# Optimization experiments

Measured on AMD Instinct MI355X. Metric: run time of the kernel, lower is better.

The kernel has to match this reference:

```python
import jax, jax.numpy as jnp
import numpy as np

B, C, H, W = 32, 64, 32, 32
DIM = H * W          # number of tokens (pixels)
DEPTH = 8
TAU = 1.0
NUM_CLASSES = 10


def setup_inputs() -> dict:
    key = jax.random.key(0)
    ks = jax.random.split(key, 6)
    return {
        "image": jax.random.normal(ks[0], (B, C, H, W), dtype=jnp.float32),
        "WV": 10.0 * jax.random.normal(ks[1], (C, C), dtype=jnp.float32),
        "WK": jax.random.normal(ks[2], (C, C), dtype=jnp.float32),
        "WQ": jax.random.normal(ks[3], (C, C), dtype=jnp.float32),
        "last_W": jax.random.normal(ks[4], (NUM_CLASSES, DIM), dtype=jnp.float32) / np.sqrt(DIM),
        "last_b": jnp.zeros((NUM_CLASSES,), dtype=jnp.float32),
    }


def reference(image, WV, WK, WQ, last_W, last_b):
    # flatten(2).transpose(1,2): (B,C,H,W) -> (B, H*W, C)
    X = image.reshape(B, C, DIM).transpose(0, 2, 1)
    scale = DIM ** (-0.5)
    for _ in range(DEPTH):
        # weight_sharing=True, sign=0 -> W = WV every layer
        Q = X @ WQ                                  # (B, n, C)
        K = X @ WK                                  # (B, n, C)
        scores = jnp.einsum('bnc,bmc->bnm', Q, K) * scale  # (B, n, n)
        A = jax.nn.softmax(scores, axis=-1)
        # diffusion_step (method 'A'): tau * A @ (X @ W) + X
        X = TAU * jnp.einsum('bnm,bmc->bnc', A, X @ WV) + X
    # mean over channel dim -> (B, dim), then Linear(dim, num_classes)
    pred = X.mean(-1) @ last_W.T + last_b
    return pred
```

## Files before the change

### kernel.cpp

```cpp
#include <hip/hip_runtime.h>
#include <math.h>

#define BB    32
#define CCH   64
#define DIMN  1024
#define NCLS  10

typedef __attribute__((ext_vector_type(8))) short bf16x8;
typedef __attribute__((ext_vector_type(4))) float f32x4;
typedef __attribute__((ext_vector_type(4))) unsigned short us4;
typedef __attribute__((ext_vector_type(8))) unsigned short us8;

#define MFMA16(a, b, c) __builtin_amdgcn_mfma_f32_16x16x32_bf16(a, b, c, 0, 0, 0)

__device__ __forceinline__ unsigned short f2bf(float x) {
  unsigned u = __float_as_uint(x);
  unsigned r = u + 0x7fffu + ((u >> 16) & 1u);
  return (unsigned short)(r >> 16);
}
__device__ __forceinline__ float bf2f(unsigned short h) {
  return __uint_as_float(((unsigned)h) << 16);
}
__device__ __forceinline__ void split3(float x, unsigned short& h,
                                       unsigned short& m, unsigned short& l) {
  h = f2bf(x); float hf = bf2f(h);
  float r = x - hf;
  m = f2bf(r); float mf = bf2f(m);
  l = f2bf(r - mf);
}
__device__ __forceinline__ void split3_pk(float x0, float x1,
                                          unsigned& hp, unsigned& mp,
                                          unsigned& lp) {
  unsigned h, m, l;
  asm("v_cvt_pk_bf16_f32 %0, %1, %2" : "=v"(h) : "v"(x0), "v"(x1));
  const float h0 = __uint_as_float(h << 16);
  const float h1 = __uint_as_float(h & 0xffff0000u);
  const float r0 = x0 - h0, r1 = x1 - h1;
  asm("v_cvt_pk_bf16_f32 %0, %1, %2" : "=v"(m) : "v"(r0), "v"(r1));
  const float m0 = __uint_as_float(m << 16);
  const float m1 = __uint_as_float(m & 0xffff0000u);
  asm("v_cvt_pk_bf16_f32 %0, %1, %2" : "=v"(l) : "v"(r0 - m0), "v"(r1 - m1));
  hp = h; mp = m; lp = l;
}
__device__ __forceinline__ void split3_frag(const float* xv, bf16x8& fh,
                                            bf16x8& fm, bf16x8& fl) {
  union U { bf16x8 v; unsigned d[4]; } uh, um, ul;
  #pragma unroll
  for (int p = 0; p < 4; ++p)
    split3_pk(xv[2 * p], xv[2 * p + 1], uh.d[p], um.d[p], ul.d[p]);
  fh = uh.v; fm = um.v; fl = ul.v;
}
__device__ __forceinline__ bf16x8 ld16B(const unsigned short* p) {
  union { us8 u; bf16x8 v; } c;
  c.u = *(const us8*)p;
  return c.v;
}

__global__ __launch_bounds__(256) void k_transpose(const float* __restrict__ img,
                                                   float* __restrict__ X) {
  __shared__ float tile[64][65];
  const int b  = blockIdx.y;
  const int n0 = blockIdx.x * 64;
  const int tx = threadIdx.x & 63;
  const int ty = threadIdx.x >> 6;
  const float* src = img + (size_t)b * CCH * DIMN;
  #pragma unroll
  for (int c = ty; c < 64; c += 4)
    tile[c][tx] = src[(size_t)c * DIMN + n0 + tx];
  __syncthreads();
  float* dst = X + (size_t)b * DIMN * CCH;
  #pragma unroll
  for (int nn = ty; nn < 64; nn += 4)
    dst[(size_t)(n0 + nn) * CCH + tx] = tile[tx][nn];
}

__global__ __launch_bounds__(256) void k_qkv_split(
    const float* __restrict__ X,
    const float* __restrict__ WQ, const float* __restrict__ WK,
    const float* __restrict__ WV,
    float* __restrict__ Q,
    unsigned short* __restrict__ Kh, unsigned short* __restrict__ Km,
    unsigned short* __restrict__ Kl,
    unsigned short* __restrict__ VhT, unsigned short* __restrict__ VmT,
    unsigned short* __restrict__ VlT) {
  __shared__ float xs[16][64];
  __shared__ unsigned short vs[3][16][64];
  const int c  = threadIdx.x & 63;
  const int tg = threadIdx.x >> 6;
  const size_t t0 = (size_t)blockIdx.x * 16;
  #pragma unroll
  for (int r = tg; r < 16; r += 4)
    xs[r][c] = X[(t0 + r) * 64 + c];
  __syncthreads();
  float qa[4] = {0.f,0.f,0.f,0.f};
  float ka[4] = {0.f,0.f,0.f,0.f};
  float va[4] = {0.f,0.f,0.f,0.f};
  for (int j = 0; j < 64; ++j) {
    const float wq = WQ[j * 64 + c];
    const float wk = WK[j * 64 + c];
    const float wv = WV[j * 64 + c];
    #pragma unroll
    for (int r = 0; r < 4; ++r) {
      const float x = xs[tg * 4 + r][j];
      qa[r] = fmaf(x, wq, qa[r]);
      ka[r] = fmaf(x, wk, ka[r]);
      va[r] = fmaf(x, wv, va[r]);
    }
  }
  #pragma unroll
  for (int r = 0; r < 4; ++r) {
    const int t = tg * 4 + r;
    const size_t idx = (t0 + t) * 64 + c;
    Q[idx] = qa[r];
    unsigned short h, m, l;
    split3(ka[r], h, m, l);
    Kh[idx] = h; Km[idx] = m; Kl[idx] = l;
    split3(va[r], h, m, l);
    vs[0][t][c] = h; vs[1][t][c] = m; vs[2][t][c] = l;
  }
  __syncthreads();
  {
    const int row  = threadIdx.x >> 2;
    const int part = threadIdx.x & 3;
    const size_t bofs = (t0 >> 10) * ((size_t)DIMN * 64);
    const size_t kt   = (t0 & 1023) >> 5;
    const size_t tin  = (size_t)part * 8 + ((t0 & 31) >> 2);
    unsigned short* dst[3] = {VhT, VmT, VlT};
    #pragma unroll
    for (int term = 0; term < 3; ++term) {
      us4 pk;
      #pragma unroll
      for (int i = 0; i < 4; ++i) pk[i] = vs[term][part * 4 + i][row];
      *(us4*)&dst[term][bofs + kt * 2048 + (size_t)row * 32 + tin] = pk;
    }
  }
}

__global__ __launch_bounds__(256) void k_qkv_merge(
    float* __restrict__ X,
    const float* __restrict__ Mp, const float* __restrict__ Lp,
    const float* __restrict__ Op,
    const float* __restrict__ WQ, const float* __restrict__ WK,
    const float* __restrict__ WV,
    float* __restrict__ Q,
    unsigned short* __restrict__ Kh, unsigned short* __restrict__ Km,
    unsigned short* __restrict__ Kl,
    unsigned short* __restrict__ VhT, unsigned short* __restrict__ VmT,
    unsigned short* __restrict__ VlT) {
  __shared__ float xs[16][64];
  __shared__ unsigned short vs[3][16][64];
  const int c  = threadIdx.x & 63;
  const int tg = threadIdx.x >> 6;
  const size_t t0 = (size_t)blockIdx.x * 16;
  #pragma unroll
  for (int r = tg; r < 16; r += 4) {
    const size_t grow = t0 + r;
    const float m0 = Mp[grow], m1 = Mp[32768 + grow];
    const float l0 = Lp[grow], l1 = Lp[32768 + grow];
    const float mm = fmaxf(m0, m1);
    const float w0 = __expf(m0 - mm), w1 = __expf(m1 - mm);
    const float inv = 1.0f / (l0 * w0 + l1 * w1);
    const float o0 = Op[grow * 64 + c];
    const float o1 = Op[(size_t)2097152 + grow * 64 + c];
    const float xn = X[grow * 64 + c] + (o0 * w0 + o1 * w1) * inv;
    X[grow * 64 + c] = xn;
    xs[r][c] = xn;
  }
  __syncthreads();
  float qa[4] = {0.f,0.f,0.f,0.f};
  float ka[4] = {0.f,0.f,0.f,0.f};
  float va[4] = {0.f,0.f,0.f,0.f};
  for (int j = 0; j < 64; ++j) {
    const float wq = WQ[j * 64 + c];
    const float wk = WK[j * 64 + c];
    const float wv = WV[j * 64 + c];
    #pragma unroll
    for (int r = 0; r < 4; ++r) {
      const float x = xs[tg * 4 + r][j];
      qa[r] = fmaf(x, wq, qa[r]);
      ka[r] = fmaf(x, wk, ka[r]);
      va[r] = fmaf(x, wv, va[r]);
    }
  }
  #pragma unroll
  for (int r = 0; r < 4; ++r) {
    const int t = tg * 4 + r;
    const size_t idx = (t0 + t) * 64 + c;
    Q[idx] = qa[r];
    unsigned short h, m, l;
    split3(ka[r], h, m, l);
    Kh[idx] = h; Km[idx] = m; Kl[idx] = l;
    split3(va[r], h, m, l);
    vs[0][t][c] = h; vs[1][t][c] = m; vs[2][t][c] = l;
  }
  __syncthreads();
  {
    const int row  = threadIdx.x >> 2;
    const int part = threadIdx.x & 3;
    const size_t bofs = (t0 >> 10) * ((size_t)DIMN * 64);
    const size_t kt   = (t0 & 1023) >> 5;
    const size_t tin  = (size_t)part * 8 + ((t0 & 31) >> 2);
    unsigned short* dst[3] = {VhT, VmT, VlT};
    #pragma unroll
    for (int term = 0; term < 3; ++term) {
      us4 pk;
      #pragma unroll
      for (int i = 0; i < 4; ++i) pk[i] = vs[term][part * 4 + i][row];
      *(us4*)&dst[term][bofs + kt * 2048 + (size_t)row * 32 + tin] = pk;
    }
  }
}

__global__ __launch_bounds__(256, 4) void k_attn_sk(
    const float* __restrict__ Qg,
    const unsigned short* __restrict__ Kh, const unsigned short* __restrict__ Km,
    const unsigned short* __restrict__ Kl,
    const unsigned short* __restrict__ VhT, const unsigned short* __restrict__ VmT,
    const unsigned short* __restrict__ VlT,
    float* __restrict__ Mp, float* __restrict__ Lp, float* __restrict__ Op) {
  __shared__ __align__(16) unsigned short Khs[32 * 72];
  __shared__ __align__(16) unsigned short Kms[32 * 72];
  __shared__ __align__(16) unsigned short Kls[32 * 72];
  __shared__ __align__(16) unsigned short Vhs[64 * 40];
  __shared__ __align__(16) unsigned short Vms[64 * 40];
  __shared__ __align__(16) unsigned short Vls[64 * 40];

  const int tid  = threadIdx.x;
  const int w    = tid >> 6;
  const int lane = tid & 63;
  const int ln   = lane & 15;
  const int q    = lane >> 4;

  const int bid   = blockIdx.x;
  const int xcd   = bid & 7;
  const int seq   = bid >> 3;
  const int b     = xcd * 4 + (seq >> 5);
  const int local = seq & 31;
  const int half  = local >> 4;
  const int i0    = (local & 15) * 64;

  const size_t base = (size_t)b * (DIMN * 64);
  const float scale = 0.03125f;

  const int kj = tid >> 3, kg = tid & 7;
  const int vc = tid >> 2, vg = tid & 3;
  const int klo = kj * 72 + kg * 8;
  const int vlo = vc * 40 + vg * 8;

  bf16x8 qh[2], qm[2], ql[2];
  {
    const int mrow = i0 + 16 * w + ln;
    const float* qp = Qg + base + (size_t)mrow * 64 + 8 * q;
    #pragma unroll
    for (int s = 0; s < 2; ++s) {
      const float4 x0 = ((const float4*)(qp + 32 * s))[0];
      const float4 x1 = ((const float4*)(qp + 32 * s))[1];
      const float xv[8] = {x0.x, x0.y, x0.z, x0.w, x1.x, x1.y, x1.z, x1.w};
      split3_frag(xv, qh[s], qm[s], ql[s]);
    }
  }

  f32x4 O[4];
  #pragma unroll
  for (int ct = 0; ct < 4; ++ct) O[ct] = (f32x4){0.f, 0.f, 0.f, 0.f};
  float m_run = -INFINITY;
  float l_run = 0.f;

  const int kt0 = half * 16;
  for (int kt = kt0; kt < kt0 + 16; ++kt) {
    __syncthreads();

    {
      const size_t tof = base + (size_t)kt * 2048 + tid * 8;
      const us8 a0 = *(const us8*)&Kh[tof];
      const us8 a1 = *(const us8*)&Km[tof];
      const us8 a2 = *(const us8*)&Kl[tof];
      const us8 b0 = *(const us8*)&VhT[tof];
      const us8 b1 = *(const us8*)&VmT[tof];
      const us8 b2 = *(const us8*)&VlT[tof];
      *(us8*)&Khs[klo] = a0;
      *(us8*)&Kms[klo] = a1;
      *(us8*)&Kls[klo] = a2;
      *(us8*)&Vhs[vlo] = b0;
      *(us8*)&Vms[vlo] = b1;
      *(us8*)&Vls[vlo] = b2;
    }
    __syncthreads();

    f32x4 sacc[2];
    #pragma unroll
    for (int ct = 0; ct < 2; ++ct) {
      f32x4 a = (f32x4){0.f, 0.f, 0.f, 0.f};
      #pragma unroll
      for (int s = 0; s < 2; ++s) {
        const int ko = (16 * ct + ln) * 72 + 32 * s + 8 * q;
        const bf16x8 bh = ld16B(&Khs[ko]);
        const bf16x8 bm = ld16B(&Kms[ko]);
        const bf16x8 bl = ld16B(&Kls[ko]);
        a = MFMA16(bh, ql[s], a);
        a = MFMA16(bl, qh[s], a);
        a = MFMA16(bm, qm[s], a);
        a = MFMA16(bh, qm[s], a);
        a = MFMA16(bm, qh[s], a);
        a = MFMA16(bh, qh[s], a);
      }
      sacc[ct] = a;
    }

    float m8 = fmaxf(fmaxf(fmaxf(sacc[0][0], sacc[0][1]),
                           fmaxf(sacc[0][2], sacc[0][3])),
                     fmaxf(fmaxf(sacc[1][0], sacc[1][1]),
                           fmaxf(sacc[1][2], sacc[1][3])));
    m8 = fmaxf(m8, __shfl_xor(m8, 16, 64));
    m8 = fmaxf(m8, __shfl_xor(m8, 32, 64));
    const float mnew  = fmaxf(m_run, m8 * scale);
    const float alpha = __expf(m_run - mnew);
    m_run = mnew;

    float pv[8];
    float s8 = 0.f;
    #pragma unroll
    for (int ct = 0; ct < 2; ++ct) {
      #pragma unroll
      for (int r = 0; r < 4; ++r) {
        const float p = __expf(sacc[ct][r] * scale - m_run);
        pv[ct * 4 + r] = p;
        s8 += p;
      }
    }
    float sr = s8 + __shfl_xor(s8, 16, 64);
    sr = sr + __shfl_xor(sr, 32, 64);
    l_run = l_run * alpha + sr;

    const int srcb = (lane & 48) + ((lane & 48) >> 2);
    float arow[4];
    #pragma unroll
    for (int r = 0; r < 4; ++r) arow[r] = __shfl(alpha, srcb + r, 64);
    #pragma unroll
    for (int ct = 0; ct < 4; ++ct) {
      #pragma unroll
      for (int r = 0; r < 4; ++r) O[ct][r] *= arow[r];
    }

    bf16x8 ph, pm, pl;
    split3_frag(pv, ph, pm, pl);

    #pragma unroll
    for (int ct = 0; ct < 4; ++ct) {
      const int vo = (16 * ct + ln) * 40 + 8 * q;
      const bf16x8 vvh = ld16B(&Vhs[vo]);
      const bf16x8 vvm = ld16B(&Vms[vo]);
      const bf16x8 vvl = ld16B(&Vls[vo]);
      O[ct] = MFMA16(ph, vvh, O[ct]);
      O[ct] = MFMA16(ph, vvm, O[ct]);
      O[ct] = MFMA16(pm, vvh, O[ct]);
      O[ct] = MFMA16(pm, vvm, O[ct]);
      O[ct] = MFMA16(ph, vvl, O[ct]);
      O[ct] = MFMA16(pl, vvh, O[ct]);
    }
  }

  const size_t hofs = (size_t)half * (32 * 1024);
  #pragma unroll
  for (int r = 0; r < 4; ++r) {
    const int row = i0 + 16 * w + 4 * q + r;
    const size_t grow = hofs + (size_t)b * DIMN + row;
    #pragma unroll
    for (int ct = 0; ct < 4; ++ct)
      Op[grow * 64 + ln + 16 * ct] = O[ct][r];
  }
  if (q == 0) {
    const size_t tgrow = hofs + (size_t)b * DIMN + i0 + 16 * w + ln;
    Mp[tgrow] = m_run;
    Lp[tgrow] = l_run;
  }
}

__global__ __launch_bounds__(256) void k_merge_mean(
    const float* __restrict__ X,
    const float* __restrict__ Mp, const float* __restrict__ Lp,
    const float* __restrict__ Op, float* __restrict__ meanv) {
  const int c  = threadIdx.x & 63;
  const int tg = threadIdx.x >> 6;
  const size_t t0 = (size_t)blockIdx.x * 128;
  for (int i = tg; i < 128; i += 4) {
    const size_t grow = t0 + i;
    const float m0 = Mp[grow], m1 = Mp[32768 + grow];
    const float l0 = Lp[grow], l1 = Lp[32768 + grow];
    const float mm = fmaxf(m0, m1);
    const float w0 = __expf(m0 - mm), w1 = __expf(m1 - mm);
    const float inv = 1.0f / (l0 * w0 + l1 * w1);
    const float o0 = Op[grow * 64 + c];
    const float o1 = Op[(size_t)2097152 + grow * 64 + c];
    float v = X[grow * 64 + c] + (o0 * w0 + o1 * w1) * inv;
    #pragma unroll
    for (int off = 32; off > 0; off >>= 1)
      v += __shfl_down(v, off, 64);
    if (c == 0) meanv[grow] = v * (1.0f / 64.0f);
  }
}

__global__ __launch_bounds__(256) void k_head2(
    const float* __restrict__ meanv, const float* __restrict__ lW,
    const float* __restrict__ lb, float* __restrict__ out) {
  __shared__ float red[256];
  const int b   = blockIdx.x;
  const int tid = threadIdx.x;
  float acc[NCLS];
  #pragma unroll
  for (int k = 0; k < NCLS; ++k) acc[k] = 0.f;
  for (int n = tid; n < DIMN; n += 256) {
    const float m = meanv[(size_t)b * DIMN + n];
    #pragma unroll
    for (int k = 0; k < NCLS; ++k)
      acc[k] = fmaf(m, lW[k * DIMN + n], acc[k]);
  }
  for (int k = 0; k < NCLS; ++k) {
    red[tid] = acc[k];
    __syncthreads();
    for (int s = 128; s > 0; s >>= 1) {
      if (tid < s) red[tid] += red[tid + s];
      __syncthreads();
    }
    if (tid == 0) out[b * NCLS + k] = red[0] + lb[k];
    __syncthreads();
  }
}

__global__ __launch_bounds__(256) void k_attn_s(
    const float* __restrict__ Qg,
    const unsigned short* __restrict__ Kh, const unsigned short* __restrict__ Km,
    const unsigned short* __restrict__ Kl,
    const unsigned short* __restrict__ VhT, const unsigned short* __restrict__ VmT,
    const unsigned short* __restrict__ VlT,
    float* __restrict__ X, float* __restrict__ meanout) {
  __shared__ __align__(16) unsigned short Khs[32 * 72];
  __shared__ __align__(16) unsigned short Kms[32 * 72];
  __shared__ __align__(16) unsigned short Kls[32 * 72];
  __shared__ __align__(16) unsigned short Vhs[64 * 40];
  __shared__ __align__(16) unsigned short Vms[64 * 40];
  __shared__ __align__(16) unsigned short Vls[64 * 40];

  const int tid  = threadIdx.x;
  const int w    = tid >> 6;
  const int lane = tid & 63;
  const int ln   = lane & 15;
  const int q    = lane >> 4;
  const int bid = blockIdx.x;
  const int xcd = bid & 7;
  const int seq = bid >> 3;
  const int b   = xcd * 4 + (seq >> 4);
  const int i0  = (seq & 15) * 64;
  const size_t base = (size_t)b * (DIMN * 64);
  const float scale = 0.03125f;

  const int kj = tid >> 3, kg = tid & 7;
  const int vc = tid >> 2, vg = tid & 3;
  const int klo = kj * 72 + kg * 8;
  const int vlo = vc * 40 + vg * 8;

  bf16x8 qh[2], qm[2], ql[2];
  {
    const int mrow = i0 + 16 * w + ln;
    const float* qp = Qg + base + (size_t)mrow * 64 + 8 * q;
    #pragma unroll
    for (int s = 0; s < 2; ++s) {
      const float4 x0 = ((const float4*)(qp + 32 * s))[0];
      const float4 x1 = ((const float4*)(qp + 32 * s))[1];
      const float xv[8] = {x0.x, x0.y, x0.z, x0.w, x1.x, x1.y, x1.z, x1.w};
      split3_frag(xv, qh[s], qm[s], ql[s]);
    }
  }

  f32x4 O[4];
  #pragma unroll
  for (int ct = 0; ct < 4; ++ct) O[ct] = (f32x4){0.f, 0.f, 0.f, 0.f};
  float m_run = -INFINITY;
  float l_run = 0.f;

  for (int kt = 0; kt < 32; ++kt) {
    __syncthreads();
    {
      const size_t tof = base + (size_t)kt * 2048 + tid * 8;
      const us8 a0 = *(const us8*)&Kh[tof];
      const us8 a1 = *(const us8*)&Km[tof];
      const us8 a2 = *(const us8*)&Kl[tof];
      const us8 b0 = *(const us8*)&VhT[tof];
      const us8 b1 = *(const us8*)&VmT[tof];
      const us8 b2 = *(const us8*)&VlT[tof];
      *(us8*)&Khs[klo] = a0;
      *(us8*)&Kms[klo] = a1;
      *(us8*)&Kls[klo] = a2;
      *(us8*)&Vhs[vlo] = b0;
      *(us8*)&Vms[vlo] = b1;
      *(us8*)&Vls[vlo] = b2;
    }
    __syncthreads();

    f32x4 sacc[2];
    #pragma unroll
    for (int ct = 0; ct < 2; ++ct) {
      f32x4 a = (f32x4){0.f, 0.f, 0.f, 0.f};
      #pragma unroll
      for (int s = 0; s < 2; ++s) {
        const int ko = (16 * ct + ln) * 72 + 32 * s + 8 * q;
        const bf16x8 bh = ld16B(&Khs[ko]);
        const bf16x8 bm = ld16B(&Kms[ko]);
        const bf16x8 bl = ld16B(&Kls[ko]);
        a = MFMA16(bh, ql[s], a);
        a = MFMA16(bl, qh[s], a);
        a = MFMA16(bm, qm[s], a);
        a = MFMA16(bh, qm[s], a);
        a = MFMA16(bm, qh[s], a);
        a = MFMA16(bh, qh[s], a);
      }
      sacc[ct] = a;
    }

    float m8 = fmaxf(fmaxf(fmaxf(sacc[0][0], sacc[0][1]),
                           fmaxf(sacc[0][2], sacc[0][3])),
                     fmaxf(fmaxf(sacc[1][0], sacc[1][1]),
                           fmaxf(sacc[1][2], sacc[1][3])));
    m8 = fmaxf(m8, __shfl_xor(m8, 16, 64));
    m8 = fmaxf(m8, __shfl_xor(m8, 32, 64));
    const float mnew  = fmaxf(m_run, m8 * scale);
    const float alpha = __expf(m_run - mnew);
    m_run = mnew;

    float pv[8];
    float s8 = 0.f;
    #pragma unroll
    for (int ct = 0; ct < 2; ++ct) {
      #pragma unroll
      for (int r = 0; r < 4; ++r) {
        const float p = __expf(sacc[ct][r] * scale - m_run);
        pv[ct * 4 + r] = p;
        s8 += p;
      }
    }
    float sr = s8 + __shfl_xor(s8, 16, 64);
    sr = sr + __shfl_xor(sr, 32, 64);
    l_run = l_run * alpha + sr;

    const int srcb = (lane & 48) + ((lane & 48) >> 2);
    float arow[4];
    #pragma unroll
    for (int r = 0; r < 4; ++r) arow[r] = __shfl(alpha, srcb + r, 64);
    #pragma unroll
    for (int ct = 0; ct < 4; ++ct) {
      #pragma unroll
      for (int r = 0; r < 4; ++r) O[ct][r] *= arow[r];
    }

    bf16x8 ph, pm, pl;
    split3_frag(pv, ph, pm, pl);

    #pragma unroll
    for (int ct = 0; ct < 4; ++ct) {
      const int vo = (16 * ct + ln) * 40 + 8 * q;
      const bf16x8 vvh = ld16B(&Vhs[vo]);
      const bf16x8 vvm = ld16B(&Vms[vo]);
      const bf16x8 vvl = ld16B(&Vls[vo]);
      O[ct] = MFMA16(ph, vvh, O[ct]);
      O[ct] = MFMA16(ph, vvm, O[ct]);
      O[ct] = MFMA16(pm, vvh, O[ct]);
      O[ct] = MFMA16(pm, vvm, O[ct]);
      O[ct] = MFMA16(ph, vvl, O[ct]);
      O[ct] = MFMA16(pl, vvh, O[ct]);
    }
  }

  const int srcb = (lane & 48) + ((lane & 48) >> 2);
  float linv[4];
  #pragma unroll
  for (int r = 0; r < 4; ++r) linv[r] = 1.0f / __shfl(l_run, srcb + r, 64);
  #pragma unroll
  for (int r = 0; r < 4; ++r) {
    const int row = i0 + 16 * w + 4 * q + r;
    float srow = 0.f;
    #pragma unroll
    for (int ct = 0; ct < 4; ++ct) {
      float* xp = X + base + (size_t)row * 64 + ln + 16 * ct;
      const float nv = *xp + O[ct][r] * linv[r];
      *xp = nv;
      srow += nv;
    }
    if (meanout) {
      #pragma unroll
      for (int mk = 1; mk <= 8; mk <<= 1)
        srow += __shfl_xor(srow, mk, 64);
      if (ln == 0) meanout[(size_t)b * DIMN + row] = srow * (1.0f / 64.0f);
    }
  }
}

extern "C" void kernel_launch(void* const* d_in, const int* in_sizes, int n_in,
                              void* d_out, int out_size, void* d_ws, size_t ws_size,
                              hipStream_t stream) {
  const float* image = (const float*)d_in[0];
  const float* WV    = (const float*)d_in[1];
  const float* WK    = (const float*)d_in[2];
  const float* WQ    = (const float*)d_in[3];
  const float* lW    = (const float*)d_in[4];
  const float* lb    = (const float*)d_in[5];
  float* out = (float*)d_out;

  float* ws = (float*)d_ws;
  const size_t NELEM = (size_t)BB * DIMN * CCH;
  const size_t NROW  = (size_t)BB * DIMN;

  const size_t need_sk   = (7 * NELEM + 5 * NROW) * sizeof(float);
  const size_t need_fast = (5 * NELEM + NROW) * sizeof(float);

  if (ws_size >= need_sk) {
    float* X = ws;
    float* Q = ws + NELEM;
    unsigned short* Kh  = (unsigned short*)(ws + 2 * NELEM);
    unsigned short* Km  = Kh + NELEM;
    unsigned short* Kl  = Kh + 2 * NELEM;
    unsigned short* VhT = Kh + 3 * NELEM;
    unsigned short* VmT = Kh + 4 * NELEM;
    unsigned short* VlT = Kh + 5 * NELEM;
    float* Op    = ws + 5 * NELEM;
    float* Mp    = ws + 7 * NELEM;
    float* Lp    = Mp + 2 * NROW;
    float* meanv = Lp + 2 * NROW;

    k_transpose<<<dim3(DIMN / 64, BB), 256, 0, stream>>>(image, X);
    k_qkv_split<<<(BB * DIMN) / 16, 256, 0, stream>>>(
        X, WQ, WK, WV, Q, Kh, Km, Kl, VhT, VmT, VlT);
    for (int layer = 0; layer < 8; ++layer) {
      k_attn_sk<<<1024, 256, 0, stream>>>(
          Q, Kh, Km, Kl, VhT, VmT, VlT, Mp, Lp, Op);
      if (layer < 7)
        k_qkv_merge<<<(BB * DIMN) / 16, 256, 0, stream>>>(
            X, Mp, Lp, Op, WQ, WK, WV, Q, Kh, Km, Kl, VhT, VmT, VlT);
    }
    k_merge_mean<<<256, 256, 0, stream>>>(X, Mp, Lp, Op, meanv);
    k_head2<<<BB, 256, 0, stream>>>(meanv, lW, lb, out);
  } else {
    float* X = ws;
    float* Q = ws + NELEM;
    unsigned short* Kh  = (unsigned short*)(ws + 2 * NELEM);
    unsigned short* Km  = Kh + NELEM;
    unsigned short* Kl  = Kh + 2 * NELEM;
    unsigned short* VhT = Kh + 3 * NELEM;
    unsigned short* VmT = Kh + 4 * NELEM;
    unsigned short* VlT = Kh + 5 * NELEM;
    float* meanv = ws + 5 * NELEM;
    (void)need_fast;

    k_transpose<<<dim3(DIMN / 64, BB), 256, 0, stream>>>(image, X);
    for (int layer = 0; layer < 8; ++layer) {
      k_qkv_split<<<(BB * DIMN) / 16, 256, 0, stream>>>(
          X, WQ, WK, WV, Q, Kh, Km, Kl, VhT, VmT, VlT);
      k_attn_s<<<512, 256, 0, stream>>>(
          Q, Kh, Km, Kl, VhT, VmT, VlT, X, (layer == 7) ? meanv : nullptr);
    }
    k_head2<<<BB, 256, 0, stream>>>(meanv, lW, lb, out);
  }
}
```

Before: 716.4 us.

## Load K/V fragments directly from global memory, dropping LDS staging and barriers

Both attention kernels now read the split bf16 K and V tiles straight from global memory into MFMA fragments instead of staging them in shared memory behind two __syncthreads per tile. This removes the LDS round-trip and the per-iteration block barriers. The cost is that each of the four waves fetches the same K/V data separately, relying on L1/L2 caching, and the global loads sit right before the MFMAs that use them, so their latency is harder to hide. k_attn_s also gets a launch-bounds occupancy hint of 4 blocks.

```diff
diff --git a/kernel.cpp b/kernel.cpp
--- a/kernel.cpp
+++ b/kernel.cpp
@@ -218,13 +218,6 @@
     const unsigned short* __restrict__ VhT, const unsigned short* __restrict__ VmT,
     const unsigned short* __restrict__ VlT,
     float* __restrict__ Mp, float* __restrict__ Lp, float* __restrict__ Op) {
-  __shared__ __align__(16) unsigned short Khs[32 * 72];
-  __shared__ __align__(16) unsigned short Kms[32 * 72];
-  __shared__ __align__(16) unsigned short Kls[32 * 72];
-  __shared__ __align__(16) unsigned short Vhs[64 * 40];
-  __shared__ __align__(16) unsigned short Vms[64 * 40];
-  __shared__ __align__(16) unsigned short Vls[64 * 40];
-
   const int tid  = threadIdx.x;
   const int w    = tid >> 6;
   const int lane = tid & 63;
@@ -242,11 +235,6 @@
   const size_t base = (size_t)b * (DIMN * 64);
   const float scale = 0.03125f;
 
-  const int kj = tid >> 3, kg = tid & 7;
-  const int vc = tid >> 2, vg = tid & 3;
-  const int klo = kj * 72 + kg * 8;
-  const int vlo = vc * 40 + vg * 8;
-
   bf16x8 qh[2], qm[2], ql[2];
   {
     const int mrow = i0 + 16 * w + ln;
@@ -268,24 +256,7 @@
 
   const int kt0 = half * 16;
   for (int kt = kt0; kt < kt0 + 16; ++kt) {
-    __syncthreads();
-
-    {
-      const size_t tof = base + (size_t)kt * 2048 + tid * 8;
-      const us8 a0 = *(const us8*)&Kh[tof];
-      const us8 a1 = *(const us8*)&Km[tof];
-      const us8 a2 = *(const us8*)&Kl[tof];
-      const us8 b0 = *(const us8*)&VhT[tof];
-      const us8 b1 = *(const us8*)&VmT[tof];
-      const us8 b2 = *(const us8*)&VlT[tof];
-      *(us8*)&Khs[klo] = a0;
-      *(us8*)&Kms[klo] = a1;
-      *(us8*)&Kls[klo] = a2;
-      *(us8*)&Vhs[vlo] = b0;
-      *(us8*)&Vms[vlo] = b1;
-      *(us8*)&Vls[vlo] = b2;
-    }
-    __syncthreads();
+    const size_t kb = base + (size_t)kt * 2048;
 
     f32x4 sacc[2];
     #pragma unroll
@@ -293,10 +264,10 @@
       f32x4 a = (f32x4){0.f, 0.f, 0.f, 0.f};
       #pragma unroll
       for (int s = 0; s < 2; ++s) {
-        const int ko = (16 * ct + ln) * 72 + 32 * s + 8 * q;
-        const bf16x8 bh = ld16B(&Khs[ko]);
-        const bf16x8 bm = ld16B(&Kms[ko]);
-        const bf16x8 bl = ld16B(&Kls[ko]);
+        const size_t ko = kb + (size_t)(16 * ct + ln) * 64 + 32 * s + 8 * q;
+        const bf16x8 bh = ld16B(&Kh[ko]);
+        const bf16x8 bm = ld16B(&Km[ko]);
+        const bf16x8 bl = ld16B(&Kl[ko]);
         a = MFMA16(bh, ql[s], a);
         a = MFMA16(bl, qh[s], a);
         a = MFMA16(bm, qm[s], a);
@@ -347,10 +318,10 @@
 
     #pragma unroll
     for (int ct = 0; ct < 4; ++ct) {
-      const int vo = (16 * ct + ln) * 40 + 8 * q;
-      const bf16x8 vvh = ld16B(&Vhs[vo]);
-      const bf16x8 vvm = ld16B(&Vms[vo]);
-      const bf16x8 vvl = ld16B(&Vls[vo]);
+      const size_t vo = kb + (size_t)(16 * ct + ln) * 32 + 8 * q;
+      const bf16x8 vvh = ld16B(&VhT[vo]);
+      const bf16x8 vvm = ld16B(&VmT[vo]);
+      const bf16x8 vvl = ld16B(&VlT[vo]);
       O[ct] = MFMA16(ph, vvh, O[ct]);
       O[ct] = MFMA16(ph, vvm, O[ct]);
       O[ct] = MFMA16(pm, vvh, O[ct]);
@@ -427,20 +398,13 @@
   }
 }
 
-__global__ __launch_bounds__(256) void k_attn_s(
+__global__ __launch_bounds__(256, 4) void k_attn_s(
     const float* __restrict__ Qg,
     const unsigned short* __restrict__ Kh, const unsigned short* __restrict__ Km,
     const unsigned short* __restrict__ Kl,
     const unsigned short* __restrict__ VhT, const unsigned short* __restrict__ VmT,
     const unsigned short* __restrict__ VlT,
     float* __restrict__ X, float* __restrict__ meanout) {
-  __shared__ __align__(16) unsigned short Khs[32 * 72];
-  __shared__ __align__(16) unsigned short Kms[32 * 72];
-  __shared__ __align__(16) unsigned short Kls[32 * 72];
-  __shared__ __align__(16) unsigned short Vhs[64 * 40];
-  __shared__ __align__(16) unsigned short Vms[64 * 40];
-  __shared__ __align__(16) unsigned short Vls[64 * 40];
-
   const int tid  = threadIdx.x;
   const int w    = tid >> 6;
   const int lane = tid & 63;
@@ -454,11 +418,6 @@
   const size_t base = (size_t)b * (DIMN * 64);
   const float scale = 0.03125f;
 
-  const int kj = tid >> 3, kg = tid & 7;
-  const int vc = tid >> 2, vg = tid & 3;
-  const int klo = kj * 72 + kg * 8;
-  const int vlo = vc * 40 + vg * 8;
-
   bf16x8 qh[2], qm[2], ql[2];
   {
     const int mrow = i0 + 16 * w + ln;
@@ -479,23 +438,7 @@
   float l_run = 0.f;
 
   for (int kt = 0; kt < 32; ++kt) {
-    __syncthreads();
-    {
-      const size_t tof = base + (size_t)kt * 2048 + tid * 8;
-      const us8 a0 = *(const us8*)&Kh[tof];
-      const us8 a1 = *(const us8*)&Km[tof];
-      const us8 a2 = *(const us8*)&Kl[tof];
-      const us8 b0 = *(const us8*)&VhT[tof];
-      const us8 b1 = *(const us8*)&VmT[tof];
-      const us8 b2 = *(const us8*)&VlT[tof];
-      *(us8*)&Khs[klo] = a0;
-      *(us8*)&Kms[klo] = a1;
-      *(us8*)&Kls[klo] = a2;
-      *(us8*)&Vhs[vlo] = b0;
-      *(us8*)&Vms[vlo] = b1;
-      *(us8*)&Vls[vlo] = b2;
-    }
-    __syncthreads();
+    const size_t kb = base + (size_t)kt * 2048;
 
     f32x4 sacc[2];
     #pragma unroll
@@ -503,10 +446,10 @@
       f32x4 a = (f32x4){0.f, 0.f, 0.f, 0.f};
       #pragma unroll
       for (int s = 0; s < 2; ++s) {
-        const int ko = (16 * ct + ln) * 72 + 32 * s + 8 * q;
-        const bf16x8 bh = ld16B(&Khs[ko]);
-        const bf16x8 bm = ld16B(&Kms[ko]);
-        const bf16x8 bl = ld16B(&Kls[ko]);
+        const size_t ko = kb + (size_t)(16 * ct + ln) * 64 + 32 * s + 8 * q;
+        const bf16x8 bh = ld16B(&Kh[ko]);
+        const bf16x8 bm = ld16B(&Km[ko]);
+        const bf16x8 bl = ld16B(&Kl[ko]);
         a = MFMA16(bh, ql[s], a);
         a = MFMA16(bl, qh[s], a);
         a = MFMA16(bm, qm[s], a);
@@ -557,10 +500,10 @@
 
     #pragma unroll
     for (int ct = 0; ct < 4; ++ct) {
-      const int vo = (16 * ct + ln) * 40 + 8 * q;
-      const bf16x8 vvh = ld16B(&Vhs[vo]);
-      const bf16x8 vvm = ld16B(&Vms[vo]);
-      const bf16x8 vvl = ld16B(&Vls[vo]);
+      const size_t vo = kb + (size_t)(16 * ct + ln) * 32 + 8 * q;
+      const bf16x8 vvh = ld16B(&VhT[vo]);
+      const bf16x8 vvm = ld16B(&VmT[vo]);
+      const bf16x8 vvl = ld16B(&VlT[vo]);
       O[ct] = MFMA16(ph, vvh, O[ct]);
       O[ct] = MFMA16(ph, vvm, O[ct]);
       O[ct] = MFMA16(pm, vvh, O[ct]);
```

Result: slower. 1.360 ms (+89.8%).
